# Performance work log

Hardware: AMD Instinct MI355X
Metric: run time of the kernel (lower is better)

## Reference

```python
import jax, jax.numpy as jnp
import numpy as np

EPS = 1e-7
FEAT_DIM = 128
N_DATA = 100000
NCE_K = 16384
NCE_T = 0.07


def _l2norm(x):
    # Normalize(power=2): x / (sum(x^2, axis=1)^(1/2))
    return x / jnp.sqrt(jnp.sum(x * x, axis=1, keepdims=True))


def _embed(x, W, b):
    return _l2norm(x @ W.T + b)


def _contrast_loss(x, n_data):
    # x: [B, K+1] of (unnormalized) probabilities; col 0 = positive
    bsz = x.shape[0]
    m = x.shape[1] - 1
    Pn = 1.0 / float(n_data)
    c = m * Pn + EPS
    log_D1 = jnp.log(x[:, 0] / (x[:, 0] + c))          # positives
    log_D0 = jnp.log((m * Pn) / (x[:, 1:] + c))         # negatives
    return -(log_D1.sum() + log_D0.sum()) / bsz


def setup_inputs() -> dict:
    key = jax.random.key(0)
    ks = jax.random.split(key, 10)
    s_dim, t_dim = 1024, 2048
    B = 64
    stdv = 1.0 / np.sqrt(FEAT_DIM / 3.0)
    inp = {
        "f_s": jax.random.normal(ks[0], (B, s_dim), dtype=jnp.float32),
        "f_t": jax.random.normal(ks[1], (B, t_dim), dtype=jnp.float32),
        "idx": jax.random.randint(ks[2], (B,), 0, N_DATA),
        "contrast_idx": jax.random.randint(ks[3], (B, NCE_K + 1), 0, N_DATA),
        # Embed params (linear): Linear(dim_in, feat_dim)
        "Ws": jax.random.normal(ks[4], (FEAT_DIM, s_dim), dtype=jnp.float32) / np.sqrt(s_dim),
        "bs": jnp.zeros((FEAT_DIM,), dtype=jnp.float32),
        "Wt": jax.random.normal(ks[5], (FEAT_DIM, t_dim), dtype=jnp.float32) / np.sqrt(t_dim),
        "bt": jnp.zeros((FEAT_DIM,), dtype=jnp.float32),
        # memory banks, init uniform(-stdv, stdv) as in CRD ContrastMemory
        "memory_v1": jax.random.uniform(ks[6], (N_DATA, FEAT_DIM), jnp.float32, -stdv, stdv),
        "memory_v2": jax.random.uniform(ks[7], (N_DATA, FEAT_DIM), jnp.float32, -stdv, stdv),
    }
    return inp


def reference(f_s, f_t, idx, contrast_idx, Ws, bs, Wt, bt, memory_v1, memory_v2):
    v_s = _embed(f_s, Ws, bs)   # [B, D]
    v_t = _embed(f_t, Wt, bt)   # [B, D]

    # idx.select(1,0).copy_(y): column 0 is the positive index
    idx_all = jnp.concatenate([idx[:, None], contrast_idx[:, 1:]], axis=1)  # [B, K+1]

    # gather from memory banks + bmm similarity
    w1 = memory_v1[idx_all]   # [B, K+1, D] (v_t side bank)
    w2 = memory_v2[idx_all]   # [B, K+1, D] (v_s side bank)
    out_t = jnp.exp(jnp.einsum('bkd,bd->bk', w1, v_t) / NCE_T)  # out_v2
    out_s = jnp.exp(jnp.einsum('bkd,bd->bk', w2, v_s) / NCE_T)  # out_v1

    # Z set on first batch: Z = out.mean() * n_data (detached constant)
    Z_s = jax.lax.stop_gradient(out_s.mean()) * N_DATA
    Z_t = jax.lax.stop_gradient(out_t.mean()) * N_DATA
    out_s = out_s / Z_s
    out_t = out_t / Z_t

    s_loss = _contrast_loss(out_s, N_DATA)
    t_loss = _contrast_loss(out_t, N_DATA)
    return s_loss + t_loss
```

## Files before the change

### kernel.cpp

```cpp
#include <hip/hip_runtime.h>

#define NDATA 100000
#define KP1 16385
#define BSZ 64
#define PTOT (BSZ * KP1)
#define NCHUNKS 6250
#define INV_T (1.0f / 0.07f)

typedef short short8 __attribute__((ext_vector_type(8)));
typedef float f32x4 __attribute__((ext_vector_type(4)));

__device__ __forceinline__ float wave_reduce64(float v) {
    #pragma unroll
    for (int off = 32; off >= 1; off >>= 1) v += __shfl_xor(v, off);
    return v;
}

__device__ __forceinline__ unsigned short f2bf(float f) {
    unsigned u = __float_as_uint(f);
    u += 0x7FFFu + ((u >> 16) & 1u);
    return (unsigned short)(u >> 16);
}

__device__ __forceinline__ short8 pack_bf16(float4 lo, float4 hi) {
    short8 r;
    r[0] = (short)f2bf(lo.x); r[1] = (short)f2bf(lo.y);
    r[2] = (short)f2bf(lo.z); r[3] = (short)f2bf(lo.w);
    r[4] = (short)f2bf(hi.x); r[5] = (short)f2bf(hi.y);
    r[6] = (short)f2bf(hi.z); r[7] = (short)f2bf(hi.w);
    return r;
}

__device__ __forceinline__ float dot4(float4 a, float4 b, float acc) {
    acc = fmaf(a.x, b.x, acc);
    acc = fmaf(a.y, b.y, acc);
    acc = fmaf(a.z, b.z, acc);
    return fmaf(a.w, b.w, acc);
}

__global__ __launch_bounds__(256) void embed_kernel(
    const float* __restrict__ fs, const float* __restrict__ ft,
    const float* __restrict__ Ws, const float* __restrict__ bs,
    const float* __restrict__ Wt, const float* __restrict__ bt,
    float* __restrict__ vraw_s, float* __restrict__ vraw_t,
    float* __restrict__ n2s, float* __restrict__ n2t)
{
    __shared__ __align__(16) float4 FS[512];
    __shared__ __align__(16) float4 FT[1024];

    const int t  = threadIdx.x;
    const int dt = blockIdx.x;
    const int b0 = blockIdx.y * 2;

    for (int q = t; q < 512; q += 256) {
        const int b = q >> 8, i = q & 255;
        FS[q] = ((const float4*)(fs + (size_t)(b0 + b) * 1024))[i];
    }
    for (int q = t; q < 1024; q += 256) {
        const int b = q >> 9, i = q & 511;
        FT[q] = ((const float4*)(ft + (size_t)(b0 + b) * 2048))[i];
    }
    __syncthreads();

    const int w = t >> 6, lane = t & 63;
    float ps0 = 0.0f, ps1 = 0.0f, pt0 = 0.0f, pt1 = 0.0f;

    #pragma unroll
    for (int r = 0; r < 4; ++r) {
        const int d = dt * 16 + w * 4 + r;
        const float4* wrow = (const float4*)(Ws + (size_t)d * 1024);
        float a0 = 0.0f, a1 = 0.0f;
        #pragma unroll
        for (int i = 0; i < 4; ++i) {
            const float4 wv = wrow[i * 64 + lane];
            a0 = dot4(wv, FS[i * 64 + lane], a0);
            a1 = dot4(wv, FS[256 + i * 64 + lane], a1);
        }
        a0 = wave_reduce64(a0) + bs[d];
        a1 = wave_reduce64(a1) + bs[d];
        ps0 = fmaf(a0, a0, ps0);
        ps1 = fmaf(a1, a1, ps1);
        if (lane == 0) {
            vraw_s[(size_t)b0 * 128 + d]       = a0;
            vraw_s[(size_t)(b0 + 1) * 128 + d] = a1;
        }
    }
    #pragma unroll
    for (int r = 0; r < 4; ++r) {
        const int d = dt * 16 + w * 4 + r;
        const float4* wrow = (const float4*)(Wt + (size_t)d * 2048);
        float a0 = 0.0f, a1 = 0.0f;
        #pragma unroll
        for (int i = 0; i < 8; ++i) {
            const float4 wv = wrow[i * 64 + lane];
            a0 = dot4(wv, FT[i * 64 + lane], a0);
            a1 = dot4(wv, FT[512 + i * 64 + lane], a1);
        }
        a0 = wave_reduce64(a0) + bt[d];
        a1 = wave_reduce64(a1) + bt[d];
        pt0 = fmaf(a0, a0, pt0);
        pt1 = fmaf(a1, a1, pt1);
        if (lane == 0) {
            vraw_t[(size_t)b0 * 128 + d]       = a0;
            vraw_t[(size_t)(b0 + 1) * 128 + d] = a1;
        }
    }
    if (lane == 0) {
        atomicAdd(&n2s[b0],     ps0);
        atomicAdd(&n2s[b0 + 1], ps1);
        atomicAdd(&n2t[b0],     pt0);
        atomicAdd(&n2t[b0 + 1], pt1);
    }
}

__global__ __launch_bounds__(256) void sgemm_kernel(
    const float* __restrict__ m1, const float* __restrict__ m2,
    const float* __restrict__ vraw_s, const float* __restrict__ vraw_t,
    float* __restrict__ S1, float* __restrict__ S2)
{
    const int t = threadIdx.x;
    const int bank = blockIdx.y;
    const float* __restrict__ bankp = bank ? m2 : m1;
    const float* __restrict__ vp    = bank ? vraw_s : vraw_t;
    float* __restrict__ Sp          = bank ? S2 : S1;

    const int lane = t & 63;
    const int m  = lane & 15;
    const int q4 = lane >> 4;

    short8 bf[4][4];
    #pragma unroll
    for (int n = 0; n < 4; ++n) {
        const float4* vrow = (const float4*)(vp + (size_t)(n * 16 + m) * 128);
        #pragma unroll
        for (int kk = 0; kk < 4; ++kk) {
            const float4 lo = vrow[(kk * 4 + q4) * 2];
            const float4 hi = vrow[(kk * 4 + q4) * 2 + 1];
            bf[n][kk] = pack_bf16(lo, hi);
        }
    }

    const int wave   = (blockIdx.x << 2) | (t >> 6);
    const int nwaves = gridDim.x << 2;

    for (int cid = wave; cid < NCHUNKS; cid += nwaves) {
        const int row0 = cid << 4;
        const float4* arow = (const float4*)(bankp + (size_t)(row0 + m) * 128);

        float4 a[8];
        #pragma unroll
        for (int kk = 0; kk < 4; ++kk) {
            a[kk * 2]     = arow[(kk * 4 + q4) * 2];
            a[kk * 2 + 1] = arow[(kk * 4 + q4) * 2 + 1];
        }
        short8 af[4];
        #pragma unroll
        for (int kk = 0; kk < 4; ++kk)
            af[kk] = pack_bf16(a[kk * 2], a[kk * 2 + 1]);

        float* __restrict__ Spage = Sp + (size_t)row0 * 64;
        #pragma unroll
        for (int n = 0; n < 4; ++n) {
            f32x4 acc = {0.f, 0.f, 0.f, 0.f};
            #pragma unroll
            for (int kk = 0; kk < 4; ++kk)
                acc = __builtin_amdgcn_mfma_f32_16x16x32_bf16(bf[n][kk], af[kk], acc, 0, 0, 0);
            *(f32x4*)(Spage + (size_t)m * 64 + n * 16 + q4 * 4) = acc;
        }
    }
}

__global__ __launch_bounds__(256) void gather_kernel(
    const int* __restrict__ cidx,
    const float* __restrict__ S1, const float* __restrict__ S2,
    const float* __restrict__ n2t, const float* __restrict__ n2s,
    float* __restrict__ acc)
{
    const int b = blockIdx.x, part = blockIdx.y, t = threadIdx.x;
    const float sct = INV_T * rsqrtf(n2t[b]);
    const float scs = INV_T * rsqrtf(n2s[b]);
    const float* __restrict__ S1b = S1 + b;
    const float* __restrict__ S2b = S2 + b;
    const int kbase = part * 1024 + 1;

    int rows[4];
    #pragma unroll
    for (int j = 0; j < 4; ++j)
        rows[j] = cidx[(size_t)b * KP1 + kbase + j * 256 + t];

    float v1[4], v2[4];
    #pragma unroll
    for (int j = 0; j < 4; ++j) {
        v1[j] = S1b[(size_t)rows[j] * 64];
        v2[j] = S2b[(size_t)rows[j] * 64];
    }

    float seT = 0.f, se2T = 0.f, seS = 0.f, se2S = 0.f;
    #pragma unroll
    for (int j = 0; j < 4; ++j) {
        const float e1 = __expf(v1[j] * sct);
        const float e2 = __expf(v2[j] * scs);
        seT += e1; se2T = fmaf(e1, e1, se2T);
        seS += e2; se2S = fmaf(e2, e2, se2S);
    }

    seT = wave_reduce64(seT);  se2T = wave_reduce64(se2T);
    seS = wave_reduce64(seS);  se2S = wave_reduce64(se2S);

    __shared__ float red[4][4];
    if ((t & 63) == 0) {
        const int w = t >> 6;
        red[w][0] = seT; red[w][1] = se2T; red[w][2] = seS; red[w][3] = se2S;
    }
    __syncthreads();
    if (t < 4)
        atomicAdd(&acc[t], red[0][t] + red[1][t] + red[2][t] + red[3][t]);
}

__global__ __launch_bounds__(64) void final_kernel(
    const int* __restrict__ idx,
    const float* __restrict__ S1, const float* __restrict__ S2,
    const float* __restrict__ n2t, const float* __restrict__ n2s,
    const float* __restrict__ acc, float* __restrict__ out)
{
    const int b = threadIdx.x;
    const float c = 0.16384f + 1e-7f;
    const int row = idx[b];

    const float e1p = __expf(S1[(size_t)row * 64 + b] * INV_T * rsqrtf(n2t[b]));
    const float e2p = __expf(S2[(size_t)row * 64 + b] * INV_T * rsqrtf(n2s[b]));

    const float pseT = wave_reduce64(e1p);
    const float pseS = wave_reduce64(e2p);

    const float seT_neg = acc[0], se2T_neg = acc[1];
    const float seS_neg = acc[2], se2S_neg = acc[3];

    const float zn = (float)PTOT / (float)NDATA;
    const float invZt = zn / (seT_neg + pseT);
    const float invZs = zn / (seS_neg + pseS);

    const float PB = (float)(PTOT - BSZ);
    const float LOG_MPN_C = -6.1035156e-7f;
    const float ic = 1.0f / c;

    const float negT = PB * LOG_MPN_C
                     - seT_neg * invZt * ic
                     + 0.5f * se2T_neg * invZt * invZt * ic * ic;
    const float negS = PB * LOG_MPN_C
                     - seS_neg * invZs * ic
                     + 0.5f * se2S_neg * invZs * invZs * ic * ic;

    const float x0t = e1p * invZt, x0s = e2p * invZs;
    float pos = __logf(x0t / (x0t + c)) + __logf(x0s / (x0s + c));
    pos = wave_reduce64(pos);

    if (b == 0) out[0] = -(negT + negS + pos) * (1.0f / 64.0f);
}

extern "C" void kernel_launch(void* const* d_in, const int* in_sizes, int n_in,
                              void* d_out, int out_size, void* d_ws, size_t ws_size,
                              hipStream_t stream) {
    const float* fs   = (const float*)d_in[0];
    const float* ft   = (const float*)d_in[1];
    const int*   idx  = (const int*)d_in[2];
    const int*   cidx = (const int*)d_in[3];
    const float* Ws   = (const float*)d_in[4];
    const float* bs   = (const float*)d_in[5];
    const float* Wt   = (const float*)d_in[6];
    const float* bt   = (const float*)d_in[7];
    const float* m1   = (const float*)d_in[8];
    const float* m2   = (const float*)d_in[9];
    float* out = (float*)d_out;

    float* ws     = (float*)d_ws;
    float* n2t    = ws;
    float* n2s    = ws + 64;
    float* acc    = ws + 128;
    float* vraw_s = ws + 144;
    float* vraw_t = vraw_s + 8192;
    float* S1     = vraw_t + 8192;
    float* S2     = S1 + (size_t)BSZ * NDATA;

    hipMemsetAsync(ws, 0, 144 * sizeof(float), stream);

    embed_kernel<<<dim3(8, 32), dim3(256), 0, stream>>>(
        fs, ft, Ws, bs, Wt, bt, vraw_s, vraw_t, n2s, n2t);
    sgemm_kernel<<<dim3(768, 2), dim3(256), 0, stream>>>(
        m1, m2, vraw_s, vraw_t, S1, S2);
    gather_kernel<<<dim3(64, 16), dim3(256), 0, stream>>>(
        cidx, S1, S2, n2t, n2s, acc);
    final_kernel<<<dim3(1), dim3(64), 0, stream>>>(
        idx, S1, S2, n2t, n2s, acc, out);
}
```

Baseline: 224.6 us.

## Fuse exp-sum into dense GEMM via per-row batch bitmask, drop score matrices

Instead of writing full 64x100000 score matrices S1/S2 and gathering them afterwards, a mask kernel builds a per-row 64-bit bitmask of which batch entries sample each memory row. The GEMM kernel then applies exp and accumulates sum and sum-of-squares in place, weighted by the mask. Duplicate samples go to an overflow list that a separate kernel recomputes with bf16-rounded dot products, and the positives are recomputed directly in the final kernel. This removes roughly 51 MB of score writes plus the scattered gather. In exchange it adds atomicOr traffic, a larger memset and extra launches, and overflow entries beyond OVF_CAP are silently dropped.

```diff
diff --git a/kernel.cpp b/kernel.cpp
--- a/kernel.cpp
+++ b/kernel.cpp
@@ -6,6 +6,8 @@
 #define PTOT (BSZ * KP1)
 #define NCHUNKS 6250
 #define INV_T (1.0f / 0.07f)
+#define OVF_CAP 256
+#define NMBLK 1024
 
 typedef short short8 __attribute__((ext_vector_type(8)));
 typedef float f32x4 __attribute__((ext_vector_type(4)));
@@ -13,6 +15,12 @@
 __device__ __forceinline__ float wave_reduce64(float v) {
     #pragma unroll
     for (int off = 32; off >= 1; off >>= 1) v += __shfl_xor(v, off);
+    return v;
+}
+
+__device__ __forceinline__ float group_reduce16(float v) {
+    v += __shfl_xor(v, 8); v += __shfl_xor(v, 4);
+    v += __shfl_xor(v, 2); v += __shfl_xor(v, 1);
     return v;
 }
 
@@ -20,6 +28,10 @@
     unsigned u = __float_as_uint(f);
     u += 0x7FFFu + ((u >> 16) & 1u);
     return (unsigned short)(u >> 16);
+}
+
+__device__ __forceinline__ float bfm(float x) {
+    return __uint_as_float(((unsigned)f2bf(x)) << 16);
 }
 
 __device__ __forceinline__ short8 pack_bf16(float4 lo, float4 hi) {
@@ -38,6 +50,18 @@
     return fmaf(a.w, b.w, acc);
 }
 
+__device__ __forceinline__ float dot8bf(const float4* a, const float4* v, int li, float d) {
+    #pragma unroll
+    for (int h = 0; h < 2; ++h) {
+        const float4 x = a[li * 2 + h], y = v[li * 2 + h];
+        d = fmaf(bfm(x.x), bfm(y.x), d);
+        d = fmaf(bfm(x.y), bfm(y.y), d);
+        d = fmaf(bfm(x.z), bfm(y.z), d);
+        d = fmaf(bfm(x.w), bfm(y.w), d);
+    }
+    return d;
+}
+
 __global__ __launch_bounds__(256) void embed_kernel(
     const float* __restrict__ fs, const float* __restrict__ ft,
     const float* __restrict__ Ws, const float* __restrict__ bs,
@@ -49,7 +73,6 @@
     __shared__ __align__(16) float4 FT[1024];
 
     const int t  = threadIdx.x;
-    const int dt = blockIdx.x;
     const int b0 = blockIdx.y * 2;
 
     for (int q = t; q < 512; q += 256) {
@@ -63,11 +86,9 @@
     __syncthreads();
 
     const int w = t >> 6, lane = t & 63;
-    float ps0 = 0.0f, ps1 = 0.0f, pt0 = 0.0f, pt1 = 0.0f;
-
-    #pragma unroll
-    for (int r = 0; r < 4; ++r) {
-        const int d = dt * 16 + w * 4 + r;
+    const int d = blockIdx.x * 4 + w;
+
+    {
         const float4* wrow = (const float4*)(Ws + (size_t)d * 1024);
         float a0 = 0.0f, a1 = 0.0f;
         #pragma unroll
@@ -78,16 +99,14 @@
         }
         a0 = wave_reduce64(a0) + bs[d];
         a1 = wave_reduce64(a1) + bs[d];
-        ps0 = fmaf(a0, a0, ps0);
-        ps1 = fmaf(a1, a1, ps1);
         if (lane == 0) {
             vraw_s[(size_t)b0 * 128 + d]       = a0;
             vraw_s[(size_t)(b0 + 1) * 128 + d] = a1;
-        }
-    }
-    #pragma unroll
-    for (int r = 0; r < 4; ++r) {
-        const int d = dt * 16 + w * 4 + r;
+            atomicAdd(&n2s[b0],     a0 * a0);
+            atomicAdd(&n2s[b0 + 1], a1 * a1);
+        }
+    }
+    {
         const float4* wrow = (const float4*)(Wt + (size_t)d * 2048);
         float a0 = 0.0f, a1 = 0.0f;
         #pragma unroll
@@ -98,37 +117,62 @@
         }
         a0 = wave_reduce64(a0) + bt[d];
         a1 = wave_reduce64(a1) + bt[d];
-        pt0 = fmaf(a0, a0, pt0);
-        pt1 = fmaf(a1, a1, pt1);
         if (lane == 0) {
             vraw_t[(size_t)b0 * 128 + d]       = a0;
             vraw_t[(size_t)(b0 + 1) * 128 + d] = a1;
-        }
-    }
-    if (lane == 0) {
-        atomicAdd(&n2s[b0],     ps0);
-        atomicAdd(&n2s[b0 + 1], ps1);
-        atomicAdd(&n2t[b0],     pt0);
-        atomicAdd(&n2t[b0 + 1], pt1);
-    }
+            atomicAdd(&n2t[b0],     a0 * a0);
+            atomicAdd(&n2t[b0 + 1], a1 * a1);
+        }
+    }
+}
+
+__global__ __launch_bounds__(256) void mask_kernel(
+    const int* __restrict__ cidx,
+    unsigned long long* __restrict__ rowmask,
+    unsigned* __restrict__ ovfcnt, unsigned* __restrict__ ovf)
+{
+    const int b = blockIdx.x, part = blockIdx.y, t = threadIdx.x;
+    __shared__ unsigned lcnt;
+    __shared__ unsigned lbuf[OVF_CAP];
+    if (t == 0) lcnt = 0;
+    __syncthreads();
+
+    const unsigned long long bit = 1ull << b;
+    const int kbase = part * 1024 + 1;
+    #pragma unroll
+    for (int j = 0; j < 4; ++j) {
+        const int row = cidx[(size_t)b * KP1 + kbase + j * 256 + t];
+        const unsigned long long old = atomicOr(&rowmask[row], bit);
+        if (old & bit) {
+            const unsigned p = atomicAdd(&lcnt, 1u);
+            if (p < OVF_CAP) lbuf[p] = ((unsigned)b << 17) | (unsigned)row;
+        }
+    }
+    __syncthreads();
+    const int blk = b * 16 + part;
+    const unsigned n = min(lcnt, (unsigned)OVF_CAP);
+    if (t == 0) ovfcnt[blk] = n;
+    for (unsigned q = t; q < n; q += 256) ovf[(size_t)blk * OVF_CAP + q] = lbuf[q];
 }
 
 __global__ __launch_bounds__(256) void sgemm_kernel(
     const float* __restrict__ m1, const float* __restrict__ m2,
     const float* __restrict__ vraw_s, const float* __restrict__ vraw_t,
-    float* __restrict__ S1, float* __restrict__ S2)
+    const float* __restrict__ n2t, const float* __restrict__ n2s,
+    const unsigned long long* __restrict__ rowmask,
+    float* __restrict__ acc)
 {
     const int t = threadIdx.x;
     const int bank = blockIdx.y;
     const float* __restrict__ bankp = bank ? m2 : m1;
     const float* __restrict__ vp    = bank ? vraw_s : vraw_t;
-    float* __restrict__ Sp          = bank ? S2 : S1;
+    const float* __restrict__ n2p   = bank ? n2s : n2t;
 
     const int lane = t & 63;
     const int m  = lane & 15;
     const int q4 = lane >> 4;
 
-    short8 bf[4][4];
+    short8 bfv[4][4];
     #pragma unroll
     for (int n = 0; n < 4; ++n) {
         const float4* vrow = (const float4*)(vp + (size_t)(n * 16 + m) * 128);
@@ -136,9 +180,19 @@
         for (int kk = 0; kk < 4; ++kk) {
             const float4 lo = vrow[(kk * 4 + q4) * 2];
             const float4 hi = vrow[(kk * 4 + q4) * 2 + 1];
-            bf[n][kk] = pack_bf16(lo, hi);
-        }
-    }
+            bfv[n][kk] = pack_bf16(lo, hi);
+        }
+    }
+
+    f32x4 scv[4];
+    #pragma unroll
+    for (int n = 0; n < 4; ++n) {
+        const f32x4 nn = ((const f32x4*)n2p)[n * 4 + q4];
+        #pragma unroll
+        for (int j = 0; j < 4; ++j) scv[n][j] = INV_T * rsqrtf(nn[j]);
+    }
+
+    float se = 0.0f, se2 = 0.0f;
 
     const int wave   = (blockIdx.x << 2) | (t >> 6);
     const int nwaves = gridDim.x << 2;
@@ -158,104 +212,145 @@
         for (int kk = 0; kk < 4; ++kk)
             af[kk] = pack_bf16(a[kk * 2], a[kk * 2 + 1]);
 
-        float* __restrict__ Spage = Sp + (size_t)row0 * 64;
+        const unsigned long long msk = rowmask[row0 + m];
+
         #pragma unroll
         for (int n = 0; n < 4; ++n) {
-            f32x4 acc = {0.f, 0.f, 0.f, 0.f};
+            f32x4 av = {0.f, 0.f, 0.f, 0.f};
             #pragma unroll
             for (int kk = 0; kk < 4; ++kk)
-                acc = __builtin_amdgcn_mfma_f32_16x16x32_bf16(bf[n][kk], af[kk], acc, 0, 0, 0);
-            *(f32x4*)(Spage + (size_t)m * 64 + n * 16 + q4 * 4) = acc;
-        }
-    }
-}
-
-__global__ __launch_bounds__(256) void gather_kernel(
-    const int* __restrict__ cidx,
-    const float* __restrict__ S1, const float* __restrict__ S2,
+                av = __builtin_amdgcn_mfma_f32_16x16x32_bf16(bfv[n][kk], af[kk], av, 0, 0, 0);
+            const int base_b = n * 16 + q4 * 4;
+            #pragma unroll
+            for (int j = 0; j < 4; ++j) {
+                const float mj = (float)((unsigned)((msk >> (base_b + j)) & 1ull));
+                const float e = __expf(av[j] * scv[n][j]) * mj;
+                se += e;
+                se2 = fmaf(e, e, se2);
+            }
+        }
+    }
+
+    se  = wave_reduce64(se);
+    se2 = wave_reduce64(se2);
+    __shared__ float red[4][2];
+    if (lane == 0) { red[t >> 6][0] = se; red[t >> 6][1] = se2; }
+    __syncthreads();
+    if (t < 2) {
+        const float s = red[0][t] + red[1][t] + red[2][t] + red[3][t];
+        atomicAdd(&acc[(blockIdx.x & 7) * 4 + bank * 2 + t], s);
+    }
+}
+
+__global__ __launch_bounds__(256) void ovf_kernel(
+    const unsigned* __restrict__ ovfcnt, const unsigned* __restrict__ ovf,
+    const float* __restrict__ m1, const float* __restrict__ m2,
+    const float* __restrict__ vraw_t, const float* __restrict__ vraw_s,
     const float* __restrict__ n2t, const float* __restrict__ n2s,
     float* __restrict__ acc)
 {
-    const int b = blockIdx.x, part = blockIdx.y, t = threadIdx.x;
-    const float sct = INV_T * rsqrtf(n2t[b]);
-    const float scs = INV_T * rsqrtf(n2s[b]);
-    const float* __restrict__ S1b = S1 + b;
-    const float* __restrict__ S2b = S2 + b;
-    const int kbase = part * 1024 + 1;
-
-    int rows[4];
-    #pragma unroll
-    for (int j = 0; j < 4; ++j)
-        rows[j] = cidx[(size_t)b * KP1 + kbase + j * 256 + t];
-
-    float v1[4], v2[4];
-    #pragma unroll
-    for (int j = 0; j < 4; ++j) {
-        v1[j] = S1b[(size_t)rows[j] * 64];
-        v2[j] = S2b[(size_t)rows[j] * 64];
-    }
+    const int blk = blockIdx.x, t = threadIdx.x;
+    const int cnt = (int)ovfcnt[blk];
+    const int wave = t >> 6, lane = t & 63, g = lane >> 4, li = lane & 15;
 
     float seT = 0.f, se2T = 0.f, seS = 0.f, se2S = 0.f;
-    #pragma unroll
-    for (int j = 0; j < 4; ++j) {
-        const float e1 = __expf(v1[j] * sct);
-        const float e2 = __expf(v2[j] * scs);
-        seT += e1; se2T = fmaf(e1, e1, se2T);
-        seS += e2; se2S = fmaf(e2, e2, se2S);
+
+    for (int i0 = 0; i0 * 16 < cnt; ++i0) {
+        const int e = i0 * 16 + wave * 4 + g;
+        const bool ok = e < cnt;
+        const unsigned ue = ovf[(size_t)blk * OVF_CAP + (ok ? e : 0)];
+        const int b = (int)(ue >> 17), row = (int)(ue & 0x1FFFFu);
+
+        float dT = dot8bf((const float4*)(m1 + (size_t)row * 128),
+                          (const float4*)(vraw_t + (size_t)b * 128), li, 0.f);
+        float dS = dot8bf((const float4*)(m2 + (size_t)row * 128),
+                          (const float4*)(vraw_s + (size_t)b * 128), li, 0.f);
+        dT = group_reduce16(dT);
+        dS = group_reduce16(dS);
+        if (ok && li == 0) {
+            const float eT = __expf(dT * INV_T * rsqrtf(n2t[b]));
+            const float eS = __expf(dS * INV_T * rsqrtf(n2s[b]));
+            seT += eT; se2T = fmaf(eT, eT, se2T);
+            seS += eS; se2S = fmaf(eS, eS, se2S);
+        }
     }
 
     seT = wave_reduce64(seT);  se2T = wave_reduce64(se2T);
     seS = wave_reduce64(seS);  se2S = wave_reduce64(se2S);
-
     __shared__ float red[4][4];
-    if ((t & 63) == 0) {
-        const int w = t >> 6;
-        red[w][0] = seT; red[w][1] = se2T; red[w][2] = seS; red[w][3] = se2S;
+    if (lane == 0) {
+        red[wave][0] = seT; red[wave][1] = se2T; red[wave][2] = seS; red[wave][3] = se2S;
     }
     __syncthreads();
     if (t < 4)
-        atomicAdd(&acc[t], red[0][t] + red[1][t] + red[2][t] + red[3][t]);
-}
-
-__global__ __launch_bounds__(64) void final_kernel(
+        atomicAdd(&acc[(blk & 7) * 4 + t], red[0][t] + red[1][t] + red[2][t] + red[3][t]);
+}
+
+__global__ __launch_bounds__(256) void final_kernel(
     const int* __restrict__ idx,
-    const float* __restrict__ S1, const float* __restrict__ S2,
+    const float* __restrict__ m1, const float* __restrict__ m2,
+    const float* __restrict__ vraw_t, const float* __restrict__ vraw_s,
     const float* __restrict__ n2t, const float* __restrict__ n2s,
     const float* __restrict__ acc, float* __restrict__ out)
 {
-    const int b = threadIdx.x;
-    const float c = 0.16384f + 1e-7f;
-    const int row = idx[b];
-
-    const float e1p = __expf(S1[(size_t)row * 64 + b] * INV_T * rsqrtf(n2t[b]));
-    const float e2p = __expf(S2[(size_t)row * 64 + b] * INV_T * rsqrtf(n2s[b]));
-
-    const float pseT = wave_reduce64(e1p);
-    const float pseS = wave_reduce64(e2p);
-
-    const float seT_neg = acc[0], se2T_neg = acc[1];
-    const float seS_neg = acc[2], se2S_neg = acc[3];
-
-    const float zn = (float)PTOT / (float)NDATA;
-    const float invZt = zn / (seT_neg + pseT);
-    const float invZs = zn / (seS_neg + pseS);
-
-    const float PB = (float)(PTOT - BSZ);
-    const float LOG_MPN_C = -6.1035156e-7f;
-    const float ic = 1.0f / c;
-
-    const float negT = PB * LOG_MPN_C
-                     - seT_neg * invZt * ic
-                     + 0.5f * se2T_neg * invZt * invZt * ic * ic;
-    const float negS = PB * LOG_MPN_C
-                     - seS_neg * invZs * ic
-                     + 0.5f * se2S_neg * invZs * invZs * ic * ic;
-
-    const float x0t = e1p * invZt, x0s = e2p * invZs;
-    float pos = __logf(x0t / (x0t + c)) + __logf(x0s / (x0s + c));
-    pos = wave_reduce64(pos);
-
-    if (b == 0) out[0] = -(negT + negS + pos) * (1.0f / 64.0f);
+    const int t = threadIdx.x, wave = t >> 6, lane = t & 63, g = lane >> 4, li = lane & 15;
+    __shared__ float e1s[64], e2s[64];
+
+    #pragma unroll
+    for (int i = 0; i < 4; ++i) {
+        const int b = wave * 16 + i * 4 + g;
+        const int row = idx[b];
+        float dT = dot8bf((const float4*)(m1 + (size_t)row * 128),
+                          (const float4*)(vraw_t + (size_t)b * 128), li, 0.f);
+        float dS = dot8bf((const float4*)(m2 + (size_t)row * 128),
+                          (const float4*)(vraw_s + (size_t)b * 128), li, 0.f);
+        dT = group_reduce16(dT);
+        dS = group_reduce16(dS);
+        if (li == 0) {
+            e1s[b] = __expf(dT * INV_T * rsqrtf(n2t[b]));
+            e2s[b] = __expf(dS * INV_T * rsqrtf(n2s[b]));
+        }
+    }
+    __syncthreads();
+
+    if (t < 64) {
+        const int b = t;
+        const float c = 0.16384f + 1e-7f;
+        const float e1p = e1s[b], e2p = e2s[b];
+
+        const float pseT = wave_reduce64(e1p);
+        const float pseS = wave_reduce64(e2p);
+
+        float seT_neg = 0.f, se2T_neg = 0.f, seS_neg = 0.f, se2S_neg = 0.f;
+        #pragma unroll
+        for (int s = 0; s < 8; ++s) {
+            seT_neg  += acc[s * 4 + 0];
+            se2T_neg += acc[s * 4 + 1];
+            seS_neg  += acc[s * 4 + 2];
+            se2S_neg += acc[s * 4 + 3];
+        }
+
+        const float zn = (float)PTOT / (float)NDATA;
+        const float invZt = zn / (seT_neg + pseT);
+        const float invZs = zn / (seS_neg + pseS);
+
+        const float PB = (float)(PTOT - BSZ);
+        const float LOG_MPN_C = -6.1035156e-7f;
+        const float ic = 1.0f / c;
+
+        const float negT = PB * LOG_MPN_C
+                         - seT_neg * invZt * ic
+                         + 0.5f * se2T_neg * invZt * invZt * ic * ic;
+        const float negS = PB * LOG_MPN_C
+                         - seS_neg * invZs * ic
+                         + 0.5f * se2S_neg * invZs * invZs * ic * ic;
+
+        const float x0t = e1p * invZt, x0s = e2p * invZs;
+        float pos = __logf(x0t / (x0t + c)) + __logf(x0s / (x0s + c));
+        pos = wave_reduce64(pos);
+
+        if (b == 0) out[0] = -(negT + negS + pos) * (1.0f / 64.0f);
+    }
 }
 
 extern "C" void kernel_launch(void* const* d_in, const int* in_sizes, int n_in,
@@ -277,19 +372,22 @@
     float* n2t    = ws;
     float* n2s    = ws + 64;
     float* acc    = ws + 128;
-    float* vraw_s = ws + 144;
+    unsigned long long* rowmask = (unsigned long long*)(ws + 256);
+    unsigned* ovfcnt = (unsigned*)(ws + 200256);
+    unsigned* ovf    = (unsigned*)(ws + 201280);
+    float* vraw_s = ws + 201280 + (size_t)NMBLK * OVF_CAP;
     float* vraw_t = vraw_s + 8192;
-    float* S1     = vraw_t + 8192;
-    float* S2     = S1 + (size_t)BSZ * NDATA;
-
-    hipMemsetAsync(ws, 0, 144 * sizeof(float), stream);
-
-    embed_kernel<<<dim3(8, 32), dim3(256), 0, stream>>>(
+
+    hipMemsetAsync(ws, 0, (size_t)(256 + 200000 + 1024) * sizeof(float), stream);
+
+    embed_kernel<<<dim3(32, 32), dim3(256), 0, stream>>>(
         fs, ft, Ws, bs, Wt, bt, vraw_s, vraw_t, n2s, n2t);
-    sgemm_kernel<<<dim3(768, 2), dim3(256), 0, stream>>>(
-        m1, m2, vraw_s, vraw_t, S1, S2);
-    gather_kernel<<<dim3(64, 16), dim3(256), 0, stream>>>(
-        cidx, S1, S2, n2t, n2s, acc);
-    final_kernel<<<dim3(1), dim3(64), 0, stream>>>(
-        idx, S1, S2, n2t, n2s, acc, out);
-}
+    mask_kernel<<<dim3(64, 16), dim3(256), 0, stream>>>(
+        cidx, rowmask, ovfcnt, ovf);
+    sgemm_kernel<<<dim3(512, 2), dim3(256), 0, stream>>>(
+        m1, m2, vraw_s, vraw_t, n2t, n2s, rowmask, acc);
+    ovf_kernel<<<dim3(NMBLK), dim3(256), 0, stream>>>(
+        ovfcnt, ovf, m1, m2, vraw_t, vraw_s, n2t, n2s, acc);
+    final_kernel<<<dim3(1), dim3(256), 0, stream>>>(
+        idx, m1, m2, vraw_t, vraw_s, n2t, n2s, acc, out);
+}
```

New measurement: 298.3 us. +32.8%, slower.
